# Performance work log

Hardware: AMD Instinct MI355X
Metric: run time of the kernel (lower is better)

## Reference

```python
import jax, jax.numpy as jnp
import numpy as np

N_NODES = 20000
N_EDGES = 320000
F_DIM = 64      # num_features == hidden_units
HID = 64
N_RUNS = 10
N_GRAPHS = 128
N_CLASSES = 10
N_LAYERS = 4
BN_EPS = 1e-5
P_DROP = 0.2


def _batchnorm(t, g, b):
    # training-mode BatchNorm1d over the flattened (num_runs*N, d) rows, biased variance
    mu = jnp.mean(t, axis=0)
    var = jnp.mean(jnp.square(t - mu), axis=0)
    return (t - mu) * jax.lax.rsqrt(var + BN_EPS) * g + b


def setup_inputs() -> dict:
    key = jax.random.key(0)
    ks = jax.random.split(key, 16)
    x = jax.random.normal(ks[0], (N_NODES, F_DIM), jnp.float32)
    edge_index = jax.random.randint(ks[1], (2, N_EDGES), 0, N_NODES, dtype=jnp.int32)
    batch = jnp.sort(jax.random.randint(ks[2], (N_NODES,), 0, N_GRAPHS, dtype=jnp.int32))
    drop_mask = jax.random.uniform(ks[3], (N_RUNS, N_NODES)) < P_DROP
    s = 0.1
    conv_w1 = jax.random.normal(ks[4], (N_LAYERS, F_DIM, HID), jnp.float32) * s
    conv_b1 = jax.random.normal(ks[5], (N_LAYERS, HID), jnp.float32) * s
    bn1_g = jax.random.uniform(ks[6], (N_LAYERS, HID), jnp.float32, 0.5, 1.5)
    bn1_b = jax.random.normal(ks[7], (N_LAYERS, HID), jnp.float32) * s
    conv_w2 = jax.random.normal(ks[8], (N_LAYERS, HID, HID), jnp.float32) * s
    conv_b2 = jax.random.normal(ks[9], (N_LAYERS, HID), jnp.float32) * s
    bn_g = jax.random.uniform(ks[10], (N_LAYERS, HID), jnp.float32, 0.5, 1.5)
    bn_b = jax.random.normal(ks[11], (N_LAYERS, HID), jnp.float32) * s
    fc_w = jax.random.normal(ks[12], (N_LAYERS + 1, HID, N_CLASSES), jnp.float32) * s
    fc_b = jax.random.normal(ks[13], (N_LAYERS + 1, N_CLASSES), jnp.float32) * s
    return dict(x=x, edge_index=edge_index, batch=batch, drop_mask=drop_mask,
                conv_w1=conv_w1, conv_b1=conv_b1, bn1_g=bn1_g, bn1_b=bn1_b,
                conv_w2=conv_w2, conv_b2=conv_b2, bn_g=bn_g, bn_b=bn_b,
                fc_w=fc_w, fc_b=fc_b)


def reference(x, edge_index, batch, drop_mask,
              conv_w1, conv_b1, bn1_g, bn1_b, conv_w2, conv_b2, bn_g, bn_b,
              fc_w, fc_b):
    # prediction path (eval): node-drop, 4 GIN layers over num_runs replicated
    # graphs, per-level mean-over-runs + global_add_pool + fc, sum, log_softmax.
    R = drop_mask.shape[0]
    N = x.shape[0]
    src, dst = edge_index[0], edge_index[1]
    # replicated node features with stochastic node drop: [R, N, F]
    h = jnp.where(drop_mask[..., None], jnp.zeros((), x.dtype), x[None])
    outs = [h]
    for i in range(N_LAYERS):
        # GINConv (eps=0): MLP(x + sum_{j->i} x_j); vectorized over runs
        # (equivalent to the original offset-replicated run_edge_index).
        agg = jnp.zeros_like(h).at[:, dst].add(h[:, src])  # [R, N, d]
        z = (h + agg).reshape(R * N, -1)
        t = z @ conv_w1[i] + conv_b1[i]
        t = jax.nn.relu(_batchnorm(t, bn1_g[i], bn1_b[i]))
        t = t @ conv_w2[i] + conv_b2[i]
        t = jax.nn.relu(_batchnorm(t, bn_g[i], bn_b[i]))
        h = t.reshape(R, N, -1)
        outs.append(h)
    out = jnp.zeros((N_GRAPHS, N_CLASSES), x.dtype)
    for i, o in enumerate(outs):
        m = jnp.mean(o, axis=0)  # [N, d] mean over runs
        pooled = jax.ops.segment_sum(m, batch, num_segments=N_GRAPHS)  # global_add_pool
        out = out + pooled @ fc_w[i] + fc_b[i]  # dropout is identity in eval
    return jax.nn.log_softmax(out, axis=-1)
```

## Files before the change

kernel.cpp:

```cpp
#include <hip/hip_runtime.h>

#define N_NODES 20000
#define N_EDGES 320000
#define R_RUNS 10
#define HID 64
#define NG 128
#define NC 10
#define NL 4
#define MROWS (R_RUNS * N_NODES)
#define BN_EPS 1e-5f
#define NCOPY 16
#define TS 72
#define AG_NPB 8
#define G2_TILES 5
#define PB_NPB 16
#define PB_SLOTS 4
#define P0_NPB 32
#define P0_SLOTS 6

typedef __bf16 bf16;
typedef __attribute__((ext_vector_type(8))) __bf16 bf16x8;
typedef __attribute__((ext_vector_type(4))) float f32x4;
typedef unsigned int uint32;

__device__ inline float blo(uint32 u) { return __uint_as_float(u << 16); }
__device__ inline float bhi(uint32 u) { return __uint_as_float(u & 0xFFFF0000u); }

constexpr size_t OFF_FLAGS   = 0;
constexpr size_t OFF_CURSOR  = 256;
constexpr size_t OFF_STATS   = 80640;
constexpr size_t OFF_POOLED5 = 146176;
constexpr size_t ZERO_BYTES  = 310016;
constexpr size_t OFF_ROWST   = 310016;
constexpr size_t OFF_COL     = 390400;
constexpr size_t OFF_KB      = 1670400;
constexpr size_t OFF_PARAMS  = 1750528;
constexpr size_t OFF_XB      = 1825792;
constexpr size_t OFF_H       = 4385792;
constexpr size_t OFF_Z       = 29985792;

#define PW1  0
#define PB1  16384
#define PG1  16640
#define PBB1 16896
#define PW2  17152
#define PB2  33536
#define PG2  33792
#define PBB2 34048
#define PFW  34304
#define PFB  37504
#define PTOT 37554
#define CVT_TOT (1280000 + PTOT)

__global__ void detect_kernel(const unsigned short* __restrict__ xu,
                              const unsigned int* __restrict__ mw,
                              int* __restrict__ cnts) {
    int tid = blockIdx.x * 256 + threadIdx.x;
    int insane = 0, lowp = 0, f32w = 0, gt1 = 0;
    for (int i = tid; i < 4096; i += 16384) {
        unsigned int u = xu[2 * i];
        if (((u >> 7) & 0xFFu) >= 0x90u) insane++;
    }
    for (int i = tid; i < 50000; i += 16384) {
        unsigned int w = mw[i];
        if ((w & 0xFFFFu) == 0x3F80u) lowp = 1;
        else if (w == 0x3F800000u) f32w = 1;
        else if (w > 1u) gt1 = 1;
    }
    if (insane) atomicAdd(&cnts[0], insane);
    if (lowp)   atomicOr(&cnts[1], 1);
    if (f32w)   atomicOr(&cnts[2], 1);
    if (gt1)    atomicOr(&cnts[3], 1);
}

__device__ inline bf16 ld_any(const void* p, int i, int f32mode) {
    if (f32mode) return (bf16)((const float*)p)[i];
    return ((const bf16*)p)[i];
}

__device__ inline int mask_dropped(const void* maskp, const int* cnts, size_t idx) {
    int w = cnts[1] ? 2 : (cnts[2] ? 4 : (cnts[3] ? 1 : 4));
    if (w == 1) return ((const unsigned char*)maskp)[idx] != 0;
    if (w == 2) return ((const unsigned short*)maskp)[idx] != 0;
    return ((const unsigned int*)maskp)[idx] != 0;
}

__global__ void convert_kernel(const int* __restrict__ cnts,
                               const void* x, const void* w1, const void* b1,
                               const void* g1, const void* bb1, const void* w2,
                               const void* b2, const void* g2, const void* bb2,
                               const void* fw, const void* fb,
                               bf16* __restrict__ xb, bf16* __restrict__ params) {
    int t = blockIdx.x * 256 + threadIdx.x;
    if (t >= CVT_TOT) return;
    int f = cnts[0] > 64;
    if (t < 1280000) { xb[t] = ld_any(x, t, f); return; }
    int u = t - 1280000;
    if (u < PB1 || (u >= PW2 && u < PB2)) {
        const void* src = (u < PB1) ? w1 : w2;
        int v = (u < PB1) ? u : u - PW2;
        int layer = v >> 12, rem = v & 4095;
        int j = rem & 7, lane = (rem >> 3) & 63, ntc = rem >> 9;
        int nt = ntc >> 1, c = ntc & 1;
        int k = c * 32 + (lane >> 4) * 8 + j;
        int n = nt * 16 + (lane & 15);
        params[u] = ld_any(src, layer * 4096 + k * 64 + n, f);
        return;
    }
    const void* src; int base;
    if      (u < PG1)  { src = b1;  base = PB1; }
    else if (u < PBB1) { src = g1;  base = PG1; }
    else if (u < PW2)  { src = bb1; base = PBB1; }
    else if (u < PG2)  { src = b2;  base = PB2; }
    else if (u < PBB2) { src = g2;  base = PG2; }
    else if (u < PFW)  { src = bb2; base = PBB2; }
    else if (u < PFB)  { src = fw;  base = PFW; }
    else               { src = fb;  base = PFB; }
    params[u] = ld_any(src, u - base, f);
}

__global__ __launch_bounds__(256) void pool0_kernel(const bf16* __restrict__ xb,
                                                    const void* __restrict__ maskp,
                                                    const int* __restrict__ cnts,
                                                    const int* __restrict__ batch,
                                                    float* __restrict__ pooled,
                                                    int* __restrict__ kb) {
    __shared__ float lp[P0_SLOTS][64];
    __shared__ float lcnt[P0_NPB];
    __shared__ int gfirst;
    int tid = threadIdx.x;
    for (int i = tid; i < P0_SLOTS * 64; i += 256) ((float*)lp)[i] = 0.f;
    if (tid == 0) gfirst = batch[blockIdx.x * P0_NPB];
    if (tid < P0_NPB) {
        int n = blockIdx.x * P0_NPB + tid;
        int cnt = 0, kbv = 0;
        #pragma unroll
        for (int r = 0; r < R_RUNS; ++r) {
            int d = mask_dropped(maskp, cnts, (size_t)r * N_NODES + n);
            kbv |= d << r;
            cnt += !d;
        }
        lcnt[tid] = (float)cnt * (1.0f / R_RUNS);
        kb[n] = kbv;
    }
    __syncthreads();
    int c = tid & 7, ln = tid >> 3;
    int n = blockIdx.x * P0_NPB + ln;
    bf16x8 xv = *(const bf16x8*)(xb + (size_t)n * HID + c * 8);
    float sc = lcnt[ln];
    int g = batch[n];
    int slot = g - gfirst;
    if (slot < P0_SLOTS) {
        #pragma unroll
        for (int j = 0; j < 8; ++j)
            atomicAdd(&lp[slot][c * 8 + j], (float)xv[j] * sc);
    } else {
        #pragma unroll
        for (int j = 0; j < 8; ++j)
            atomicAdd(&pooled[g * HID + c * 8 + j], (float)xv[j] * sc);
    }
    __syncthreads();
    for (int s = tid >> 6; s < P0_SLOTS; s += 4) {
        int f = tid & 63;
        float v = lp[s][f];
        if (v != 0.f) atomicAdd(&pooled[(gfirst + s) * HID + f], v);
    }
}

__global__ void csr_count_kernel(const int* __restrict__ ei, int* __restrict__ deg) {
    int e = blockIdx.x * 256 + threadIdx.x;
    if (e < N_EDGES) atomicAdd(&deg[ei[N_EDGES + e]], 1);
}

__global__ void csr_scan_kernel(int* __restrict__ deg, int* __restrict__ row_start) {
    __shared__ int lds[1024];
    int tid = threadIdx.x;
    const int CH = 20;
    int base = tid * CH;
    int local[CH];
    int s = 0;
    #pragma unroll
    for (int j = 0; j < CH; ++j) {
        int n = base + j;
        int d = (n < N_NODES) ? deg[n] : 0;
        local[j] = d; s += d;
    }
    lds[tid] = s; __syncthreads();
    for (int off = 1; off < 1024; off <<= 1) {
        int add = (tid >= off) ? lds[tid - off] : 0;
        __syncthreads();
        lds[tid] += add;
        __syncthreads();
    }
    int excl = lds[tid] - s;
    #pragma unroll
    for (int j = 0; j < CH; ++j) {
        int n = base + j;
        if (n < N_NODES) { row_start[n] = excl; deg[n] = excl; excl += local[j]; }
    }
    if (tid == 1023) row_start[N_NODES] = lds[1023];
}

__global__ void csr_fill_kernel(const int* __restrict__ ei, int* __restrict__ cursor,
                                int* __restrict__ col) {
    int e = blockIdx.x * 256 + threadIdx.x;
    if (e < N_EDGES) {
        int src = ei[e];
        int dst = ei[N_EDGES + e];
        int pos = atomicAdd(&cursor[dst], 1);
        col[pos] = src;
    }
}

__global__ __launch_bounds__(256) void ag1_l1_kernel(const uint32* __restrict__ xbD,
                                                     const int* __restrict__ kb,
                                                     const int* __restrict__ row_start,
                                                     const int* __restrict__ col,
                                                     const bf16* __restrict__ Wf,
                                                     const bf16* __restrict__ bias,
                                                     bf16* __restrict__ out,
                                                     float* __restrict__ statsOut) {
    __shared__ __align__(16) bf16 zT[AG_NPB * R_RUNS * TS];
    __shared__ float lsum[64], lsq[64];
    uint32* zTu = (uint32*)zT;
    int tid = threadIdx.x;
    int wave = tid >> 6, lane = tid & 63, l16 = lane & 15, quad = lane >> 4;
    int p = lane & 31, hf = lane >> 5;
    int b = blockIdx.x;

    if (tid < 64) { lsum[tid] = 0.f; lsq[tid] = 0.f; }

    for (int i = 0; i < AG_NPB / 4; ++i) {
        int nl = wave + 4 * i;
        int n = b * AG_NPB + nl;
        float ax[R_RUNS], ay[R_RUNS];
        {
            uint32 xs = xbD[(size_t)n * 32 + p];
            int ms = kb[n];
            float fx = blo(xs), fy = bhi(xs);
            #pragma unroll
            for (int r = 0; r < R_RUNS; ++r) {
                int keep = (hf == 0) && !((ms >> r) & 1);
                ax[r] = keep ? fx : 0.f;
                ay[r] = keep ? fy : 0.f;
            }
        }
        int beg = row_start[n], end = row_start[n + 1];
        int iters = (end - beg + 1) >> 1;
        int k = 0;
        for (; k + 4 <= iters; k += 4) {
            uint32 xv[4]; int mv[4];
            #pragma unroll
            for (int u = 0; u < 4; ++u) {
                int idx = beg + 2 * (k + u) + hf;
                int valid = idx < end;
                int j = valid ? col[idx] : n;
                xv[u] = xbD[(size_t)j * 32 + p];
                mv[u] = valid ? kb[j] : 0x3FF;
            }
            #pragma unroll
            for (int u = 0; u < 4; ++u) {
                float fx = blo(xv[u]), fy = bhi(xv[u]);
                #pragma unroll
                for (int r = 0; r < R_RUNS; ++r)
                    if (!((mv[u] >> r) & 1)) { ax[r] += fx; ay[r] += fy; }
            }
        }
        for (; k < iters; ++k) {
            int idx = beg + 2 * k + hf;
            int valid = idx < end;
            int j = valid ? col[idx] : n;
            uint32 xv = xbD[(size_t)j * 32 + p];
            int mv = valid ? kb[j] : 0x3FF;
            float fx = blo(xv), fy = bhi(xv);
            #pragma unroll
            for (int r = 0; r < R_RUNS; ++r)
                if (!((mv >> r) & 1)) { ax[r] += fx; ay[r] += fy; }
        }
        #pragma unroll
        for (int r = 0; r < R_RUNS; ++r) {
            ax[r] += __shfl_xor(ax[r], 32);
            ay[r] += __shfl_xor(ay[r], 32);
        }
        #pragma unroll
        for (int q = 0; q < 5; ++q) {
            int r = hf * 5 + q;
            unsigned short lo = __builtin_bit_cast(unsigned short, (bf16)ax[r]);
            unsigned short hi = __builtin_bit_cast(unsigned short, (bf16)ay[r]);
            zTu[(nl * R_RUNS + r) * (TS / 2) + p] = (uint32)lo | ((uint32)hi << 16);
        }
    }
    __syncthreads();

    bf16x8 bfr[4][2];
    #pragma unroll
    for (int nt = 0; nt < 4; ++nt)
        #pragma unroll
        for (int c = 0; c < 2; ++c)
            bfr[nt][c] = *(const bf16x8*)(Wf + (size_t)((nt * 2 + c) * 64 + lane) * 8);
    float bvs[4];
    #pragma unroll
    for (int nt = 0; nt < 4; ++nt) bvs[nt] = (float)bias[nt * 16 + l16];

    for (int g = wave; g < 5; g += 4) {
        const bf16* tp = &zT[(g * 16 + l16) * TS];
        bf16x8 a0 = *(const bf16x8*)(tp + quad * 8);
        bf16x8 a1 = *(const bf16x8*)(tp + 32 + quad * 8);
        f32x4 acc[4];
        #pragma unroll
        for (int nt = 0; nt < 4; ++nt) acc[nt] = (f32x4){bvs[nt], bvs[nt], bvs[nt], bvs[nt]};
        #pragma unroll
        for (int nt = 0; nt < 4; ++nt) {
            acc[nt] = __builtin_amdgcn_mfma_f32_16x16x32_bf16(a0, bfr[nt][0], acc[nt], 0, 0, 0);
            acc[nt] = __builtin_amdgcn_mfma_f32_16x16x32_bf16(a1, bfr[nt][1], acc[nt], 0, 0, 0);
        }
        size_t rowBase = (size_t)b * (AG_NPB * R_RUNS) + g * 16;
        #pragma unroll
        for (int nt = 0; nt < 4; ++nt) {
            float ss = 0.f, qq = 0.f;
            #pragma unroll
            for (int reg = 0; reg < 4; ++reg) {
                float v = acc[nt][reg];
                ss += v; qq += v * v;
                out[(rowBase + quad * 4 + reg) * HID + nt * 16 + l16] = (bf16)v;
            }
            atomicAdd(&lsum[nt * 16 + l16], ss);
            atomicAdd(&lsq[nt * 16 + l16], qq);
        }
    }
    __syncthreads();
    if (tid < 64) {
        int copy = b & (NCOPY - 1);
        atomicAdd(&statsOut[copy * 128 + tid], lsum[tid]);
        atomicAdd(&statsOut[copy * 128 + 64 + tid], lsq[tid]);
    }
}

__global__ __launch_bounds__(512) void ag1_kernel(const uint32* __restrict__ hD,
                                                  const int* __restrict__ row_start,
                                                  const int* __restrict__ col,
                                                  const bf16* __restrict__ Wf,
                                                  const bf16* __restrict__ bias,
                                                  bf16* __restrict__ out,
                                                  float* __restrict__ statsOut) {
    __shared__ __align__(16) bf16 zT[AG_NPB * R_RUNS * TS];
    __shared__ float lsum[64], lsq[64];
    uint32* zTu = (uint32*)zT;
    int tid = threadIdx.x;
    int wave = tid >> 6, lane = tid & 63, l16 = lane & 15, quad = lane >> 4;
    int b = blockIdx.x;
    const int NODE_DW = R_RUNS * HID / 2;

    if (tid < 64) { lsum[tid] = 0.f; lsq[tid] = 0.f; }

    {
        int nl = wave;
        int n = b * AG_NPB + nl;
        size_t base4 = (size_t)n * NODE_DW + lane * 4;
        size_t baset = (size_t)n * NODE_DW + 256 + lane;
        float acc[10];
        {
            uint4 u = *(const uint4*)(hD + base4);
            uint32 tw = hD[baset];
            acc[0] = blo(u.x); acc[1] = bhi(u.x);
            acc[2] = blo(u.y); acc[3] = bhi(u.y);
            acc[4] = blo(u.z); acc[5] = bhi(u.z);
            acc[6] = blo(u.w); acc[7] = bhi(u.w);
            acc[8] = blo(tw);  acc[9] = bhi(tw);
        }
        int beg = row_start[n], end = row_start[n + 1];
        int idx = beg;
        for (; idx + 4 <= end; idx += 4) {
            uint4 a[4]; uint32 tw[4];
            #pragma unroll
            for (int u = 0; u < 4; ++u) {
                size_t o = (size_t)col[idx + u] * NODE_DW;
                a[u] = *(const uint4*)(hD + o + lane * 4);
                tw[u] = hD[o + 256 + lane];
            }
            #pragma unroll
            for (int u = 0; u < 4; ++u) {
                uint32 wd[4] = {a[u].x, a[u].y, a[u].z, a[u].w};
                #pragma unroll
                for (int c = 0; c < 4; ++c) {
                    acc[2 * c]     += blo(wd[c]);
                    acc[2 * c + 1] += bhi(wd[c]);
                }
                acc[8] += blo(tw[u]);
                acc[9] += bhi(tw[u]);
            }
        }
        for (; idx < end; ++idx) {
            size_t o = (size_t)col[idx] * NODE_DW;
            uint4 a0 = *(const uint4*)(hD + o + lane * 4);
            uint32 t0 = hD[o + 256 + lane];
            uint32 wd[4] = {a0.x, a0.y, a0.z, a0.w};
            #pragma unroll
            for (int c = 0; c < 4; ++c) {
                acc[2 * c]     += blo(wd[c]);
                acc[2 * c + 1] += bhi(wd[c]);
            }
            acc[8] += blo(t0);
            acc[9] += bhi(t0);
        }
        #pragma unroll
        for (int c = 0; c < 5; ++c) {
            int d = (c < 4) ? (lane * 4 + c) : (256 + lane);
            int rL = nl * R_RUNS + (d >> 5);
            int fp = d & 31;
            unsigned short lo = __builtin_bit_cast(unsigned short, (bf16)acc[2 * c]);
            unsigned short hi = __builtin_bit_cast(unsigned short, (bf16)acc[2 * c + 1]);
            zTu[rL * (TS / 2) + fp] = (uint32)lo | ((uint32)hi << 16);
        }
    }
    __syncthreads();

    if (wave < 5) {
        bf16x8 bfr[4][2];
        #pragma unroll
        for (int nt = 0; nt < 4; ++nt)
            #pragma unroll
            for (int c = 0; c < 2; ++c)
                bfr[nt][c] = *(const bf16x8*)(Wf + (size_t)((nt * 2 + c) * 64 + lane) * 8);
        int g = wave;
        const bf16* tp = &zT[(g * 16 + l16) * TS];
        bf16x8 a0 = *(const bf16x8*)(tp + quad * 8);
        bf16x8 a1 = *(const bf16x8*)(tp + 32 + quad * 8);
        f32x4 acc[4];
        #pragma unroll
        for (int nt = 0; nt < 4; ++nt) {
            float bv = (float)bias[nt * 16 + l16];
            acc[nt] = (f32x4){bv, bv, bv, bv};
        }
        #pragma unroll
        for (int nt = 0; nt < 4; ++nt) {
            acc[nt] = __builtin_amdgcn_mfma_f32_16x16x32_bf16(a0, bfr[nt][0], acc[nt], 0, 0, 0);
            acc[nt] = __builtin_amdgcn_mfma_f32_16x16x32_bf16(a1, bfr[nt][1], acc[nt], 0, 0, 0);
        }
        size_t rowBase = (size_t)b * (AG_NPB * R_RUNS) + g * 16;
        #pragma unroll
        for (int nt = 0; nt < 4; ++nt) {
            float ss = 0.f, qq = 0.f;
            #pragma unroll
            for (int reg = 0; reg < 4; ++reg) {
                float v = acc[nt][reg];
                ss += v; qq += v * v;
                out[(rowBase + quad * 4 + reg) * HID + nt * 16 + l16] = (bf16)v;
            }
            atomicAdd(&lsum[nt * 16 + l16], ss);
            atomicAdd(&lsq[nt * 16 + l16], qq);
        }
    }
    __syncthreads();
    if (tid < 64) {
        int copy = b & (NCOPY - 1);
        atomicAdd(&statsOut[copy * 128 + tid], lsum[tid]);
        atomicAdd(&statsOut[copy * 128 + 64 + tid], lsq[tid]);
    }
}

__global__ __launch_bounds__(256) void gemm64_kernel(const bf16* in,
                                                     const bf16* __restrict__ Wf,
                                                     const bf16* __restrict__ bias,
                                                     bf16* out,
                                                     const float* __restrict__ statsIn,
                                                     const bf16* __restrict__ gammaIn,
                                                     const bf16* __restrict__ betaIn,
                                                     float* __restrict__ statsOut) {
    __shared__ float lstat[128];
    __shared__ float lscale[64], lshift[64];
    __shared__ float lsum[64], lsq[64];
    int tid = threadIdx.x;
    int wave = tid >> 6, lane = tid & 63, l16 = lane & 15, quad = lane >> 4;

    if (tid < 128) {
        float s = 0.f;
        #pragma unroll
        for (int k = 0; k < NCOPY; ++k) s += statsIn[k * 128 + tid];
        lstat[tid] = s;
    }
    if (tid < 64) { lsum[tid] = 0.f; lsq[tid] = 0.f; }
    __syncthreads();
    if (tid < 64) {
        float mu = lstat[tid] * (1.0f / MROWS);
        float var = lstat[tid + 64] * (1.0f / MROWS) - mu * mu;
        float rs = rsqrtf(var + BN_EPS);
        float a = (float)gammaIn[tid] * rs;
        lscale[tid] = a;
        lshift[tid] = (float)betaIn[tid] - mu * a;
    }
    __syncthreads();

    bf16x8 bfrag[4][2];
    #pragma unroll
    for (int nt = 0; nt < 4; ++nt)
        #pragma unroll
        for (int c = 0; c < 2; ++c)
            bfrag[nt][c] = *(const bf16x8*)(Wf + (size_t)((nt * 2 + c) * 64 + lane) * 8);
    float bvs[4];
    #pragma unroll
    for (int nt = 0; nt < 4; ++nt) bvs[nt] = (float)bias[nt * 16 + l16];

    for (int t5 = 0; t5 < G2_TILES; ++t5) {
        size_t rowBase = (size_t)blockIdx.x * (G2_TILES * 64) + t5 * 64 + wave * 16;
        f32x4 acc[4];
        #pragma unroll
        for (int nt = 0; nt < 4; ++nt) acc[nt] = (f32x4){bvs[nt], bvs[nt], bvs[nt], bvs[nt]};

        size_t row = rowBase + l16;
        bf16x8 afrag[2];
        #pragma unroll
        for (int c = 0; c < 2; ++c) {
            int k0 = c * 32 + quad * 8;
            bf16x8 v = *(const bf16x8*)(in + row * HID + k0);
            #pragma unroll
            for (int j = 0; j < 8; ++j) {
                float f = (float)v[j] * lscale[k0 + j] + lshift[k0 + j];
                v[j] = (bf16)fmaxf(f, 0.f);
            }
            afrag[c] = v;
        }

        #pragma unroll
        for (int nt = 0; nt < 4; ++nt) {
            acc[nt] = __builtin_amdgcn_mfma_f32_16x16x32_bf16(afrag[0], bfrag[nt][0], acc[nt], 0, 0, 0);
            acc[nt] = __builtin_amdgcn_mfma_f32_16x16x32_bf16(afrag[1], bfrag[nt][1], acc[nt], 0, 0, 0);
        }

        #pragma unroll
        for (int nt = 0; nt < 4; ++nt) {
            float s = 0.f, q = 0.f;
            #pragma unroll
            for (int reg = 0; reg < 4; ++reg) {
                float v = acc[nt][reg];
                s += v; q += v * v;
                out[(rowBase + quad * 4 + reg) * HID + nt * 16 + l16] = (bf16)v;
            }
            atomicAdd(&lsum[nt * 16 + l16], s);
            atomicAdd(&lsq[nt * 16 + l16], q);
        }
    }
    __syncthreads();
    if (tid < 64) {
        int copy = blockIdx.x & (NCOPY - 1);
        atomicAdd(&statsOut[copy * 128 + tid], lsum[tid]);
        atomicAdd(&statsOut[copy * 128 + 64 + tid], lsq[tid]);
    }
}

__global__ __launch_bounds__(256) void pool_bn_kernel(const bf16* __restrict__ t,
                                                      const float* __restrict__ statsIn,
                                                      const bf16* __restrict__ gammaIn,
                                                      const bf16* __restrict__ betaIn,
                                                      bf16* __restrict__ hOut,
                                                      const int* __restrict__ batch,
                                                      float* __restrict__ pooled) {
    __shared__ float lstat[128], lscale[64], lshift[64];
    __shared__ float lp[PB_SLOTS][64];
    __shared__ int gfirst;
    int tid = threadIdx.x;
    if (tid < 128) {
        float s = 0.f;
        #pragma unroll
        for (int k = 0; k < NCOPY; ++k) s += statsIn[k * 128 + tid];
        lstat[tid] = s;
    }
    for (int i = tid; i < PB_SLOTS * 64; i += 256) ((float*)lp)[i] = 0.f;
    if (tid == 0) gfirst = batch[blockIdx.x * PB_NPB];
    __syncthreads();
    if (tid < 64) {
        float mu = lstat[tid] * (1.0f / MROWS);
        float var = lstat[tid + 64] * (1.0f / MROWS) - mu * mu;
        float rs = rsqrtf(var + BN_EPS);
        float a = (float)gammaIn[tid] * rs;
        lscale[tid] = a;
        lshift[tid] = (float)betaIn[tid] - mu * a;
    }
    __syncthreads();
    int f = tid & 63, nsub = tid >> 6;
    float sc = lscale[f], sh = lshift[f];
    #pragma unroll
    for (int j = 0; j < PB_NPB / 4; ++j) {
        int n = blockIdx.x * PB_NPB + j * 4 + nsub;
        size_t base = (size_t)n * (R_RUNS * HID) + f;
        float s = 0.f;
        #pragma unroll
        for (int r = 0; r < R_RUNS; ++r) {
            float v = (float)t[base + r * HID];
            v = fmaxf(v * sc + sh, 0.f);
            hOut[base + r * HID] = (bf16)v;
            s += v;
        }
        int g = batch[n];
        int slot = g - gfirst;
        if (slot < PB_SLOTS) atomicAdd(&lp[slot][f], s * (1.0f / R_RUNS));
        else                 atomicAdd(&pooled[g * HID + f], s * (1.0f / R_RUNS));
    }
    __syncthreads();
    for (int s = tid >> 6; s < PB_SLOTS; s += 4) {
        float v = lp[s][tid & 63];
        if (v != 0.f) atomicAdd(&pooled[(gfirst + s) * HID + (tid & 63)], v);
    }
}

__global__ void fc_softmax_kernel(const float* __restrict__ pooled5,
                                  const bf16* __restrict__ params,
                                  const int* __restrict__ cnts, void* __restrict__ out) {
    int g = threadIdx.x;
    if (g >= NG) return;
    float o[NC];
    #pragma unroll
    for (int c = 0; c < NC; ++c) o[c] = 0.f;
    for (int l = 0; l < NL + 1; ++l) {
        const float* pg = pooled5 + ((size_t)l * NG + g) * HID;
        const bf16* fw = params + PFW + l * (HID * NC);
        for (int k = 0; k < HID; ++k) {
            float p = pg[k];
            #pragma unroll
            for (int c = 0; c < NC; ++c) o[c] += p * (float)fw[k * NC + c];
        }
        #pragma unroll
        for (int c = 0; c < NC; ++c) o[c] += (float)params[PFB + l * NC + c];
    }
    float m = -1e30f;
    #pragma unroll
    for (int c = 0; c < NC; ++c) m = fmaxf(m, o[c]);
    float s = 0.f;
    #pragma unroll
    for (int c = 0; c < NC; ++c) s += expf(o[c] - m);
    float lg = logf(s);
    int f = cnts[0] > 64;
    #pragma unroll
    for (int c = 0; c < NC; ++c) {
        float val = o[c] - m - lg;
        if (f) ((float*)out)[g * NC + c] = val;
        else   ((bf16*)out)[g * NC + c] = (bf16)val;
    }
}

extern "C" void kernel_launch(void* const* d_in, const int* in_sizes, int n_in,
                              void* d_out, int out_size, void* d_ws, size_t ws_size,
                              hipStream_t stream) {
    const void* x     = d_in[0];
    const int*  ei    = (const int*)d_in[1];
    const int*  batch = (const int*)d_in[2];
    const void* maskp = d_in[3];

    char* ws = (char*)d_ws;
    int*   cnts    = (int*)(ws + OFF_FLAGS);
    int*   cursor  = (int*)(ws + OFF_CURSOR);
    float* statsb  = (float*)(ws + OFF_STATS);
    float* pooled5 = (float*)(ws + OFF_POOLED5);
    int*   rowst   = (int*)(ws + OFF_ROWST);
    int*   colbuf  = (int*)(ws + OFF_COL);
    int*   kbuf    = (int*)(ws + OFF_KB);
    bf16*  params  = (bf16*)(ws + OFF_PARAMS);
    bf16*  xb      = (bf16*)(ws + OFF_XB);
    bf16*  h       = (bf16*)(ws + OFF_H);
    bf16*  z       = (bf16*)(ws + OFF_Z);

    hipMemsetAsync(ws, 0, ZERO_BYTES, stream);

    detect_kernel<<<64, 256, 0, stream>>>((const unsigned short*)x,
                                          (const unsigned int*)maskp, cnts);
    convert_kernel<<<(CVT_TOT + 255) / 256, 256, 0, stream>>>(
        cnts, x, d_in[4], d_in[5], d_in[6], d_in[7], d_in[8], d_in[9], d_in[10],
        d_in[11], d_in[12], d_in[13], xb, params);

    csr_count_kernel<<<(N_EDGES + 255) / 256, 256, 0, stream>>>(ei, cursor);
    csr_scan_kernel<<<1, 1024, 0, stream>>>(cursor, rowst);
    csr_fill_kernel<<<(N_EDGES + 255) / 256, 256, 0, stream>>>(ei, cursor, colbuf);

    pool0_kernel<<<N_NODES / P0_NPB, 256, 0, stream>>>(xb, maskp, cnts, batch,
                                                       pooled5, kbuf);

    for (int i = 0; i < NL; ++i) {
        float* st1 = statsb + (size_t)(2 * i) * (NCOPY * 128);
        float* st2 = statsb + (size_t)(2 * i + 1) * (NCOPY * 128);

        if (i == 0) {
            ag1_l1_kernel<<<N_NODES / AG_NPB, 256, 0, stream>>>(
                (const uint32*)xb, kbuf, rowst, colbuf,
                params + PW1, params + PB1, z, st1);
        } else {
            ag1_kernel<<<N_NODES / AG_NPB, 512, 0, stream>>>(
                (const uint32*)h, rowst, colbuf,
                params + PW1 + i * 4096, params + PB1 + i * 64, z, st1);
        }

        gemm64_kernel<<<MROWS / (G2_TILES * 64), 256, 0, stream>>>(
            z, params + PW2 + i * 4096, params + PB2 + i * 64, z,
            st1, params + PG1 + i * 64, params + PBB1 + i * 64, st2);

        pool_bn_kernel<<<N_NODES / PB_NPB, 256, 0, stream>>>(
            z, st2, params + PG2 + i * 64, params + PBB2 + i * 64, h, batch,
            pooled5 + (size_t)(i + 1) * NG * HID);
    }

    fc_softmax_kernel<<<1, 128, 0, stream>>>(pooled5, params, cnts, d_out);
}
```

Measured before the change: 730.7 us.

## Fuse second BatchNorm+ReLU and pooling into next layer's aggregation kernel

Result: slower. 824.6 us (+12.8%).

```diff
diff --git a/kernel.cpp b/kernel.cpp
--- a/kernel.cpp
+++ b/kernel.cpp
@@ -12,6 +12,7 @@
 #define NCOPY 16
 #define TS 72
 #define AG_NPB 8
+#define AG_SLOTS 3
 #define G2_TILES 5
 #define PB_NPB 16
 #define PB_SLOTS 4
@@ -36,8 +37,8 @@
 constexpr size_t OFF_KB      = 1670400;
 constexpr size_t OFF_PARAMS  = 1750528;
 constexpr size_t OFF_XB      = 1825792;
-constexpr size_t OFF_H       = 4385792;
-constexpr size_t OFF_Z       = 29985792;
+constexpr size_t OFF_A       = 4385792;
+constexpr size_t OFF_B       = 29985792;
 
 #define PW1  0
 #define PB1  16384
@@ -336,37 +337,97 @@
     }
 }
 
-__global__ __launch_bounds__(512) void ag1_kernel(const uint32* __restrict__ hD,
+__global__ __launch_bounds__(512) void ag1_kernel(const uint32* __restrict__ tD,
                                                   const int* __restrict__ row_start,
                                                   const int* __restrict__ col,
                                                   const bf16* __restrict__ Wf,
                                                   const bf16* __restrict__ bias,
+                                                  const float* __restrict__ statsIn,
+                                                  const bf16* __restrict__ gammaIn,
+                                                  const bf16* __restrict__ betaIn,
+                                                  const int* __restrict__ batch,
+                                                  float* __restrict__ pooledOut,
                                                   bf16* __restrict__ out,
                                                   float* __restrict__ statsOut) {
     __shared__ __align__(16) bf16 zT[AG_NPB * R_RUNS * TS];
-    __shared__ float lsum[64], lsq[64];
+    __shared__ float lsum[64], lsq[64], lstat[128], lscale[64], lshift[64];
+    __shared__ float lp[AG_SLOTS][64];
+    __shared__ int gfirst;
     uint32* zTu = (uint32*)zT;
     int tid = threadIdx.x;
     int wave = tid >> 6, lane = tid & 63, l16 = lane & 15, quad = lane >> 4;
     int b = blockIdx.x;
     const int NODE_DW = R_RUNS * HID / 2;
 
+    if (tid < 128) {
+        float s = 0.f;
+        #pragma unroll
+        for (int k = 0; k < NCOPY; ++k) s += statsIn[k * 128 + tid];
+        lstat[tid] = s;
+    }
     if (tid < 64) { lsum[tid] = 0.f; lsq[tid] = 0.f; }
+    for (int i = tid; i < AG_SLOTS * 64; i += 512) ((float*)lp)[i] = 0.f;
+    if (tid == 0) gfirst = batch[b * AG_NPB];
+    __syncthreads();
+    if (tid < 64) {
+        float mu = lstat[tid] * (1.0f / MROWS);
+        float var = lstat[tid + 64] * (1.0f / MROWS) - mu * mu;
+        float rs = rsqrtf(var + BN_EPS);
+        float a = (float)gammaIn[tid] * rs;
+        lscale[tid] = a;
+        lshift[tid] = (float)betaIn[tid] - mu * a;
+    }
+    __syncthreads();
 
     {
         int nl = wave;
         int n = b * AG_NPB + nl;
+        float scx[5], scy[5], shx[5], shy[5];
+        #pragma unroll
+        for (int c = 0; c < 4; ++c) {
+            int f = (8 * lane + 2 * c) & 63;
+            scx[c] = lscale[f]; scy[c] = lscale[f + 1];
+            shx[c] = lshift[f]; shy[c] = lshift[f + 1];
+        }
+        {
+            int f = (2 * lane) & 63;
+            scx[4] = lscale[f]; scy[4] = lscale[f + 1];
+            shx[4] = lshift[f]; shy[4] = lshift[f + 1];
+        }
         size_t base4 = (size_t)n * NODE_DW + lane * 4;
         size_t baset = (size_t)n * NODE_DW + 256 + lane;
         float acc[10];
         {
-            uint4 u = *(const uint4*)(hD + base4);
-            uint32 tw = hD[baset];
-            acc[0] = blo(u.x); acc[1] = bhi(u.x);
-            acc[2] = blo(u.y); acc[3] = bhi(u.y);
-            acc[4] = blo(u.z); acc[5] = bhi(u.z);
-            acc[6] = blo(u.w); acc[7] = bhi(u.w);
-            acc[8] = blo(tw);  acc[9] = bhi(tw);
+            uint4 u = *(const uint4*)(tD + base4);
+            uint32 tw = tD[baset];
+            uint32 wd[4] = {u.x, u.y, u.z, u.w};
+            int g = batch[n];
+            int slot = g - gfirst;
+            #pragma unroll
+            for (int c = 0; c < 4; ++c) {
+                float vx = fmaxf(blo(wd[c]) * scx[c] + shx[c], 0.f);
+                float vy = fmaxf(bhi(wd[c]) * scy[c] + shy[c], 0.f);
+                acc[2 * c] = vx; acc[2 * c + 1] = vy;
+                int f = (8 * lane + 2 * c) & 63;
+                if (slot < AG_SLOTS) {
+                    atomicAdd(&lp[slot][f], vx);
+                    atomicAdd(&lp[slot][f + 1], vy);
+                } else {
+                    atomicAdd(&pooledOut[g * HID + f], vx * (1.0f / R_RUNS));
+                    atomicAdd(&pooledOut[g * HID + f + 1], vy * (1.0f / R_RUNS));
+                }
+            }
+            float vx = fmaxf(blo(tw) * scx[4] + shx[4], 0.f);
+            float vy = fmaxf(bhi(tw) * scy[4] + shy[4], 0.f);
+            acc[8] = vx; acc[9] = vy;
+            int f = (2 * lane) & 63;
+            if (slot < AG_SLOTS) {
+                atomicAdd(&lp[slot][f], vx);
+                atomicAdd(&lp[slot][f + 1], vy);
+            } else {
+                atomicAdd(&pooledOut[g * HID + f], vx * (1.0f / R_RUNS));
+                atomicAdd(&pooledOut[g * HID + f + 1], vy * (1.0f / R_RUNS));
+            }
         }
         int beg = row_start[n], end = row_start[n + 1];
         int idx = beg;
@@ -375,38 +436,38 @@
             #pragma unroll
             for (int u = 0; u < 4; ++u) {
                 size_t o = (size_t)col[idx + u] * NODE_DW;
-                a[u] = *(const uint4*)(hD + o + lane * 4);
-                tw[u] = hD[o + 256 + lane];
+                a[u] = *(const uint4*)(tD + o + lane * 4);
+                tw[u] = tD[o + 256 + lane];
             }
             #pragma unroll
             for (int u = 0; u < 4; ++u) {
                 uint32 wd[4] = {a[u].x, a[u].y, a[u].z, a[u].w};
                 #pragma unroll
                 for (int c = 0; c < 4; ++c) {
-                    acc[2 * c]     += blo(wd[c]);
-                    acc[2 * c + 1] += bhi(wd[c]);
+                    acc[2 * c]     += fmaxf(blo(wd[c]) * scx[c] + shx[c], 0.f);
+                    acc[2 * c + 1] += fmaxf(bhi(wd[c]) * scy[c] + shy[c], 0.f);
                 }
-                acc[8] += blo(tw[u]);
-                acc[9] += bhi(tw[u]);
+                acc[8] += fmaxf(blo(tw[u]) * scx[4] + shx[4], 0.f);
+                acc[9] += fmaxf(bhi(tw[u]) * scy[4] + shy[4], 0.f);
             }
         }
         for (; idx < end; ++idx) {
             size_t o = (size_t)col[idx] * NODE_DW;
-            uint4 a0 = *(const uint4*)(hD + o + lane * 4);
-            uint32 t0 = hD[o + 256 + lane];
+            uint4 a0 = *(const uint4*)(tD + o + lane * 4);
+            uint32 t0 = tD[o + 256 + lane];
             uint32 wd[4] = {a0.x, a0.y, a0.z, a0.w};
             #pragma unroll
             for (int c = 0; c < 4; ++c) {
-                acc[2 * c]     += blo(wd[c]);
-                acc[2 * c + 1] += bhi(wd[c]);
-            }
-            acc[8] += blo(t0);
-            acc[9] += bhi(t0);
+                acc[2 * c]     += fmaxf(blo(wd[c]) * scx[c] + shx[c], 0.f);
+                acc[2 * c + 1] += fmaxf(bhi(wd[c]) * scy[c] + shy[c], 0.f);
+            }
+            acc[8] += fmaxf(blo(t0) * scx[4] + shx[4], 0.f);
+            acc[9] += fmaxf(bhi(t0) * scy[4] + shy[4], 0.f);
         }
         #pragma unroll
         for (int c = 0; c < 5; ++c) {
             int d = (c < 4) ? (lane * 4 + c) : (256 + lane);
-            int rL = nl * R_RUNS + (d >> 5);
+            int rL = wave * R_RUNS + (d >> 5);
             int fp = d & 31;
             unsigned short lo = __builtin_bit_cast(unsigned short, (bf16)acc[2 * c]);
             unsigned short hi = __builtin_bit_cast(unsigned short, (bf16)acc[2 * c + 1]);
@@ -457,12 +518,18 @@
         atomicAdd(&statsOut[copy * 128 + tid], lsum[tid]);
         atomicAdd(&statsOut[copy * 128 + 64 + tid], lsq[tid]);
     }
-}
-
-__global__ __launch_bounds__(256) void gemm64_kernel(const bf16* in,
+    for (int i = tid; i < AG_SLOTS * 64; i += 512) {
+        float v = lp[i >> 6][i & 63];
+        if (v != 0.f)
+            atomicAdd(&pooledOut[(gfirst + (i >> 6)) * HID + (i & 63)],
+                      v * (1.0f / R_RUNS));
+    }
+}
+
+__global__ __launch_bounds__(256) void gemm64_kernel(const bf16* __restrict__ in,
                                                      const bf16* __restrict__ Wf,
                                                      const bf16* __restrict__ bias,
-                                                     bf16* out,
+                                                     bf16* __restrict__ out,
                                                      const float* __restrict__ statsIn,
                                                      const bf16* __restrict__ gammaIn,
                                                      const bf16* __restrict__ betaIn,
@@ -548,13 +615,12 @@
     }
 }
 
-__global__ __launch_bounds__(256) void pool_bn_kernel(const bf16* __restrict__ t,
-                                                      const float* __restrict__ statsIn,
-                                                      const bf16* __restrict__ gammaIn,
-                                                      const bf16* __restrict__ betaIn,
-                                                      bf16* __restrict__ hOut,
-                                                      const int* __restrict__ batch,
-                                                      float* __restrict__ pooled) {
+__global__ __launch_bounds__(256) void pool_last_kernel(const bf16* __restrict__ t,
+                                                        const float* __restrict__ statsIn,
+                                                        const bf16* __restrict__ gammaIn,
+                                                        const bf16* __restrict__ betaIn,
+                                                        const int* __restrict__ batch,
+                                                        float* __restrict__ pooled) {
     __shared__ float lstat[128], lscale[64], lshift[64];
     __shared__ float lp[PB_SLOTS][64];
     __shared__ int gfirst;
@@ -585,12 +651,8 @@
         size_t base = (size_t)n * (R_RUNS * HID) + f;
         float s = 0.f;
         #pragma unroll
-        for (int r = 0; r < R_RUNS; ++r) {
-            float v = (float)t[base + r * HID];
-            v = fmaxf(v * sc + sh, 0.f);
-            hOut[base + r * HID] = (bf16)v;
-            s += v;
-        }
+        for (int r = 0; r < R_RUNS; ++r)
+            s += fmaxf((float)t[base + r * HID] * sc + sh, 0.f);
         int g = batch[n];
         int slot = g - gfirst;
         if (slot < PB_SLOTS) atomicAdd(&lp[slot][f], s * (1.0f / R_RUNS));
@@ -656,8 +718,8 @@
     int*   kbuf    = (int*)(ws + OFF_KB);
     bf16*  params  = (bf16*)(ws + OFF_PARAMS);
     bf16*  xb      = (bf16*)(ws + OFF_XB);
-    bf16*  h       = (bf16*)(ws + OFF_H);
-    bf16*  z       = (bf16*)(ws + OFF_Z);
+    bf16*  bufA    = (bf16*)(ws + OFF_A);
+    bf16*  bufB    = (bf16*)(ws + OFF_B);
 
     hipMemsetAsync(ws, 0, ZERO_BYTES, stream);
 
@@ -681,21 +743,25 @@
         if (i == 0) {
             ag1_l1_kernel<<<N_NODES / AG_NPB, 256, 0, stream>>>(
                 (const uint32*)xb, kbuf, rowst, colbuf,
-                params + PW1, params + PB1, z, st1);
+                params + PW1, params + PB1, bufB, st1);
         } else {
+            float* st2prev = statsb + (size_t)(2 * (i - 1) + 1) * (NCOPY * 128);
             ag1_kernel<<<N_NODES / AG_NPB, 512, 0, stream>>>(
-                (const uint32*)h, rowst, colbuf,
-                params + PW1 + i * 4096, params + PB1 + i * 64, z, st1);
+                (const uint32*)bufA, rowst, colbuf,
+                params + PW1 + i * 4096, params + PB1 + i * 64,
+                st2prev, params + PG2 + (i - 1) * 64, params + PBB2 + (i - 1) * 64,
+                batch, pooled5 + (size_t)i * NG * HID, bufB, st1);
         }
 
         gemm64_kernel<<<MROWS / (G2_TILES * 64), 256, 0, stream>>>(
-            z, params + PW2 + i * 4096, params + PB2 + i * 64, z,
+            bufB, params + PW2 + i * 4096, params + PB2 + i * 64, bufA,
             st1, params + PG1 + i * 64, params + PBB1 + i * 64, st2);
-
-        pool_bn_kernel<<<N_NODES / PB_NPB, 256, 0, stream>>>(
-            z, st2, params + PG2 + i * 64, params + PBB2 + i * 64, h, batch,
-            pooled5 + (size_t)(i + 1) * NG * HID);
-    }
+    }
+
+    pool_last_kernel<<<N_NODES / PB_NPB, 256, 0, stream>>>(
+        bufA, statsb + (size_t)(2 * (NL - 1) + 1) * (NCOPY * 128),
+        params + PG2 + (NL - 1) * 64, params + PBB2 + (NL - 1) * 64,
+        batch, pooled5 + (size_t)NL * NG * HID);
 
     fc_softmax_kernel<<<1, 128, 0, stream>>>(pooled5, params, cnts, d_out);
 }
```
